# Kernel optimization log

Hardware: AMD Instinct MI355X
Metric: run time of the kernel (lower is better)

Reference implementation:

```python
import jax, jax.numpy as jnp
import numpy as np

N = 100000
E = 1000000
HID = 64


def gcn_conv(x, W, b, edge_index, edge_w, num_nodes):
    # PyG GCNConv with edge_weight: add self-loops (weight 1), symmetric norm,
    # out[c] = sum_e norm_e * (x @ W)[row_e] aggregated at col_e, plus bias.
    xw = x @ W  # [N, hid]
    row = jnp.concatenate([edge_index[0], jnp.arange(num_nodes)])
    col = jnp.concatenate([edge_index[1], jnp.arange(num_nodes)])
    ew = jnp.concatenate([edge_w, jnp.ones((num_nodes,), x.dtype)])
    deg = jax.ops.segment_sum(ew, col, num_segments=num_nodes)
    dinv = jnp.where(deg > 0, jax.lax.rsqrt(deg), 0.0)
    norm = dinv[row] * ew * dinv[col]  # [E+N]
    msgs = norm[:, None] * xw[row]  # [E+N, hid]
    out = jax.ops.segment_sum(msgs, col, num_segments=num_nodes)
    return out + b


def setup_inputs() -> dict:
    key = jax.random.key(0)
    ks = jax.random.split(key, 12)
    user_x = jax.random.normal(ks[0], (N, 3), jnp.float32)
    movie_x = jax.random.normal(ks[1], (N, 18), jnp.float32)
    edge_index = jax.random.randint(ks[2], (2, E), 0, N, jnp.int64)
    edge_attr = jax.random.uniform(ks[3], (E,), jnp.float32)
    def lin(k, fan_in, fan_out):
        bound = 1.0 / np.sqrt(fan_in)
        k1, k2 = jax.random.split(k)
        W = jax.random.uniform(k1, (fan_in, fan_out), jnp.float32, -bound, bound)
        b = jax.random.uniform(k2, (fan_out,), jnp.float32, -bound, bound)
        return W, b
    W_user, b_user = lin(ks[4], 3, HID)
    W_movie, b_movie = lin(ks[5], 18, HID)
    W1, b1 = lin(ks[6], 2 * HID, 128)
    W2, b2 = lin(ks[7], 128, 1)
    return {"user_x": user_x, "movie_x": movie_x, "edge_index": edge_index,
            "edge_attr": edge_attr, "W_user": W_user, "b_user": b_user,
            "W_movie": W_movie, "b_movie": b_movie, "W1": W1, "b1": b1,
            "W2": W2, "b2": b2}


def reference(user_x, movie_x, edge_index, edge_attr, W_user, b_user,
              W_movie, b_movie, W1, b1, W2, b2):
    user_out = gcn_conv(user_x, W_user, b_user, edge_index, edge_attr, N)
    movie_out = gcn_conv(movie_x, W_movie, b_movie, edge_index, edge_attr, N)
    h = jnp.concatenate([user_out, movie_out], axis=-1)  # [N, 128]
    h = jax.nn.relu(h @ W1 + b1)
    rating_pred = h @ W2 + b2  # [N, 1]
    return rating_pred
```

## Files before the change

### kernel.cpp

```cpp
#include <hip/hip_runtime.h>
#include <hip/hip_fp16.h>

#define NN 100000
#define NE 1000000
#define BSH 7
#define BCOLS 128
#define NBUCK 782
#define SBLK 256
#define SITER 16
#define CAP 2048
#define OVCAP 16384

__device__ __forceinline__ float2 h2f(unsigned u) {
    union { unsigned u; __half2 h; } c; c.u = u;
    return __half22float2(c.h);
}
__device__ __forceinline__ unsigned f2h2(float a, float b) {
    union { __half2 h; unsigned u; } c; c.h = __floats2half2_rn(a, b);
    return c.u;
}

#define ACC_ROW16(base)                                                      \
    {                                                                        \
        const uint4* pr_ = (const uint4*)(base);                             \
        const uint4 A_ = pr_[0];                                             \
        const uint4 B_ = pr_[1];                                             \
        const uint4 C_ = pr_[2];                                             \
        float2 f_;                                                           \
        f_ = h2f(A_.x); s21[0]  = fmaf(w, f_.x, s21[0]);  s21[1]  = fmaf(w, f_.y, s21[1]);  \
        f_ = h2f(A_.y); s21[2]  = fmaf(w, f_.x, s21[2]);  s21[3]  = fmaf(w, f_.y, s21[3]);  \
        f_ = h2f(A_.z); s21[4]  = fmaf(w, f_.x, s21[4]);  s21[5]  = fmaf(w, f_.y, s21[5]);  \
        f_ = h2f(A_.w); s21[6]  = fmaf(w, f_.x, s21[6]);  s21[7]  = fmaf(w, f_.y, s21[7]);  \
        f_ = h2f(B_.x); s21[8]  = fmaf(w, f_.x, s21[8]);  s21[9]  = fmaf(w, f_.y, s21[9]);  \
        f_ = h2f(B_.y); s21[10] = fmaf(w, f_.x, s21[10]); s21[11] = fmaf(w, f_.y, s21[11]); \
        f_ = h2f(B_.z); s21[12] = fmaf(w, f_.x, s21[12]); s21[13] = fmaf(w, f_.y, s21[13]); \
        f_ = h2f(B_.w); s21[14] = fmaf(w, f_.x, s21[14]); s21[15] = fmaf(w, f_.y, s21[15]); \
        f_ = h2f(C_.x); s21[16] = fmaf(w, f_.x, s21[16]); s21[17] = fmaf(w, f_.y, s21[17]); \
        f_ = h2f(C_.y); s21[18] = fmaf(w, f_.x, s21[18]); s21[19] = fmaf(w, f_.y, s21[19]); \
        f_ = h2f(C_.z); s21[20] = fmaf(w, f_.x, s21[20]);                    \
    }

__global__ __launch_bounds__(128) void fuse_kernel(const float* __restrict__ Wu,
                                                   const float* __restrict__ bu,
                                                   const float* __restrict__ Wm,
                                                   const float* __restrict__ bm,
                                                   const float* __restrict__ W1,
                                                   const float* __restrict__ b1,
                                                   const float* __restrict__ W2,
                                                   float* __restrict__ Mt,
                                                   int* __restrict__ gcur,
                                                   int* __restrict__ ovfn) {
    const int j = threadIdx.x;
    for (int i = j; i < NBUCK; i += 128) gcur[i] = 0;
    if (j == 0) *ovfn = 0;

    float w1c[128];
#pragma unroll
    for (int k = 0; k < 128; k++) w1c[k] = W1[k * 128 + j];

    float* row = Mt + j * 24;
#pragma unroll
    for (int m = 0; m < 3; m++) {
        float acc = 0.f;
#pragma unroll
        for (int k = 0; k < 64; k++) acc = fmaf(Wu[m * 64 + k], w1c[k], acc);
        row[m] = acc;
    }
#pragma unroll
    for (int m = 0; m < 18; m++) {
        float acc = 0.f;
#pragma unroll
        for (int k = 0; k < 64; k++) acc = fmaf(Wm[m * 64 + k], w1c[64 + k], acc);
        row[3 + m] = acc;
    }
    float bp = b1[j];
#pragma unroll
    for (int k = 0; k < 64; k++) {
        bp = fmaf(bu[k], w1c[k], bp);
        bp = fmaf(bm[k], w1c[64 + k], bp);
    }
    row[21] = bp;
    row[22] = W2[j];
    row[23] = 0.f;
}

__global__ __launch_bounds__(256) void bscatter_kernel(const int* __restrict__ ei,
                                                       const float* __restrict__ ew,
                                                       int* __restrict__ gcur,
                                                       int2* __restrict__ mid,
                                                       int4* __restrict__ ovf,
                                                       int* __restrict__ ovfn) {
    __shared__ int h[NBUCK];
    __shared__ int rbase[NBUCK];
    int cs[SITER], rs[SITER];
    float wv[SITER];
    const int e0 = blockIdx.x * 256 + threadIdx.x;

    for (int i = threadIdx.x; i < NBUCK; i += 256) h[i] = 0;
    __syncthreads();
#pragma unroll
    for (int k = 0; k < SITER; k++) {
        const int e = e0 + k * (SBLK * 256);
        if (e < NE) {
            cs[k] = ei[NE + e];
            rs[k] = ei[e];
            wv[k] = ew[e];
            atomicAdd(&h[cs[k] >> BSH], 1);
        }
    }
    __syncthreads();
    for (int i = threadIdx.x; i < NBUCK; i += 256) {
        const int c0 = h[i];
        rbase[i] = c0 ? atomicAdd(&gcur[i], c0) : 0;
        h[i] = 0;
    }
    __syncthreads();
#pragma unroll
    for (int k = 0; k < SITER; k++) {
        const int e = e0 + k * (SBLK * 256);
        if (e < NE) {
            const int bb = cs[k] >> BSH;
            const int pos = rbase[bb] + atomicAdd(&h[bb], 1);
            if (pos < CAP) {
                mid[(size_t)bb * CAP + pos] =
                    make_int2((cs[k] & (BCOLS - 1)) | (rs[k] << BSH),
                              __float_as_int(wv[k]));
            } else {
                const int oi = atomicAdd(ovfn, 1);
                if (oi < OVCAP)
                    ovf[oi] = make_int4(cs[k], rs[k], __float_as_int(wv[k]), 0);
            }
        }
    }
}

__global__ __launch_bounds__(256) void bdeg_pack_kernel(const int2* __restrict__ mid,
                                                        const int* __restrict__ gcur,
                                                        const int* __restrict__ ovfn,
                                                        const int4* __restrict__ ovf,
                                                        const float* __restrict__ ux,
                                                        const float* __restrict__ mx,
                                                        unsigned short* __restrict__ pack16,
                                                        float* __restrict__ dinv) {
    __shared__ float dl[BCOLS];
    const int b = blockIdx.x;
    const int t = threadIdx.x;
    if (t < BCOLS) dl[t] = 0.f;
    __syncthreads();
    const int cntt = gcur[b];
    const int segc = cntt < CAP ? cntt : CAP;
    const int start = b * CAP;
    for (int i = t; i < segc; i += 256) {
        const int2 p = mid[start + i];
        atomicAdd(&dl[p.x & (BCOLS - 1)], __int_as_float(p.y));
    }
    if (cntt > CAP) {
        const int n = min(*ovfn, OVCAP);
        for (int i = t; i < n; i += 256) {
            const int4 q = ovf[i];
            if ((q.x >> BSH) == b)
                atomicAdd(&dl[q.x & (BCOLS - 1)], __int_as_float(q.z));
        }
    }
    __syncthreads();
    if (t < BCOLS) {
        const int r = b * BCOLS + t;
        if (r < NN) {
            const float d = rsqrtf(dl[t] + 1.0f);
            dinv[r] = d;
            float v[22];
            const float* u = ux + (size_t)r * 3;
            const float* m = mx + (size_t)r * 18;
            v[0] = d * u[0];
            v[1] = d * u[1];
            v[2] = d * u[2];
#pragma unroll
            for (int k = 0; k < 18; k++) v[3 + k] = d * m[k];
            v[21] = d;
            unsigned wb[16];
#pragma unroll
            for (int k = 0; k < 11; k++) wb[k] = f2h2(v[2 * k], v[2 * k + 1]);
#pragma unroll
            for (int k = 11; k < 16; k++) wb[k] = 0u;
            uint4* dst = (uint4*)(pack16 + (size_t)r * 32);
            dst[0] = make_uint4(wb[0], wb[1], wb[2], wb[3]);
            dst[1] = make_uint4(wb[4], wb[5], wb[6], wb[7]);
            dst[2] = make_uint4(wb[8], wb[9], wb[10], wb[11]);
            dst[3] = make_uint4(wb[12], wb[13], wb[14], wb[15]);
        }
    }
}

__global__ __launch_bounds__(512) void bagg_mlp_kernel(const int2* __restrict__ mid,
                                                       const int* __restrict__ gcur,
                                                       const int* __restrict__ ovfn,
                                                       const int4* __restrict__ ovf,
                                                       const unsigned short* __restrict__ pack16,
                                                       const float* __restrict__ dinv,
                                                       const float* __restrict__ Mt,
                                                       const float* __restrict__ b2,
                                                       float* __restrict__ out) {
    __shared__ int2 smid[CAP];
    __shared__ int ccnt[BCOLS];
    __shared__ int cbase[BCOLS];
    __shared__ int cptr[BCOLS];
    __shared__ float sp[3][BCOLS][21];
    __shared__ float po[3][BCOLS];

    const int b = blockIdx.x;
    const int t = threadIdx.x;
    const int col = t & (BCOLS - 1);
    const int hf = t >> 7;
    const int start = b * CAP;
    const int cntt = gcur[b];
    const int segc = cntt < CAP ? cntt : CAP;

    if (t < BCOLS) ccnt[t] = 0;
    __syncthreads();
    for (int i = t; i < segc; i += 512)
        atomicAdd(&ccnt[mid[start + i].x & (BCOLS - 1)], 1);
    __syncthreads();

    if (t < 64) {
        const int a = ccnt[2 * t];
        const int bb = ccnt[2 * t + 1];
        int p = a + bb;
#pragma unroll
        for (int d = 1; d < 64; d <<= 1) {
            const int x = __shfl_up(p, d, 64);
            if (t >= d) p += x;
        }
        cbase[2 * t] = p - bb;
        cbase[2 * t + 1] = p;
        cptr[2 * t] = p - bb - a;
        cptr[2 * t + 1] = p - bb;
    }
    __syncthreads();

    for (int i = t; i < segc; i += 512) {
        const int2 p = mid[start + i];
        const int pos = atomicAdd(&cptr[p.x & (BCOLS - 1)], 1);
        smid[pos] = p;
    }
    __syncthreads();

    float s21[21];
#pragma unroll
    for (int m = 0; m < 21; m++) s21[m] = 0.f;

    const int s0 = (col == 0) ? 0 : cbase[col - 1];
    const int s1 = cbase[col];
#pragma unroll 2
    for (int i = s0 + hf; i < s1; i += 4) {
        const int2 p = smid[i];
        const unsigned row = ((unsigned)p.x) >> BSH;
        const float w = __int_as_float(p.y);
        ACC_ROW16(pack16 + (size_t)row * 32);
    }

    if (hf) {
#pragma unroll
        for (int m = 0; m < 21; m++) sp[hf - 1][col][m] = s21[m];
    }
    __syncthreads();

    const int c = b * BCOLS + col;
    if (hf == 0) {
#pragma unroll
        for (int m = 0; m < 21; m++)
            s21[m] += sp[0][col][m] + sp[1][col][m] + sp[2][col][m];
        if (cntt > CAP && c < NN) {
            const int n = min(*ovfn, OVCAP);
            for (int i = 0; i < n; i++) {
                const int4 q = ovf[i];
                if (q.x == c) {
                    const unsigned row = (unsigned)q.y;
                    const float w = __int_as_float(q.z);
                    ACC_ROW16(pack16 + (size_t)row * 32);
                }
            }
        }
        if (c < NN) {
            const float w = 1.0f;
            ACC_ROW16(pack16 + (size_t)c * 32);
            const float d = dinv[c];
#pragma unroll
            for (int m = 0; m < 21; m++) s21[m] *= d;
        }
#pragma unroll
        for (int m = 0; m < 21; m++) sp[0][col][m] = s21[m];
    }
    __syncthreads();
    if (hf) {
#pragma unroll
        for (int m = 0; m < 21; m++) s21[m] = sp[0][col][m];
    }

    float o = 0.f;
    if (c < NN) {
        const int k0 = hf * 32;
#pragma unroll 2
        for (int k = k0; k < k0 + 32; k++) {
            const float* r = Mt + k * 24;
            float hsum = r[21];
#pragma unroll
            for (int m = 0; m < 21; m++) hsum = fmaf(s21[m], r[m], hsum);
            o = fmaf(fmaxf(hsum, 0.f), r[22], o);
        }
    }
    if (hf) po[hf - 1][col] = o;
    __syncthreads();
    if (hf == 0 && c < NN)
        out[c] = o + po[0][col] + po[1][col] + po[2][col] + b2[0];
}

extern "C" void kernel_launch(void* const* d_in, const int* in_sizes, int n_in,
                              void* d_out, int out_size, void* d_ws, size_t ws_size,
                              hipStream_t stream) {
    const float* ux = (const float*)d_in[0];
    const float* mx = (const float*)d_in[1];
    const int* ei = (const int*)d_in[2];
    const float* ew = (const float*)d_in[3];
    const float* Wu = (const float*)d_in[4];
    const float* bu = (const float*)d_in[5];
    const float* Wm = (const float*)d_in[6];
    const float* bm = (const float*)d_in[7];
    const float* W1 = (const float*)d_in[8];
    const float* b1 = (const float*)d_in[9];
    const float* W2 = (const float*)d_in[10];
    const float* b2 = (const float*)d_in[11];
    float* out = (float*)d_out;

    char* ws = (char*)d_ws;
    int*            gcur   = (int*)ws;
    int*            ovfn   = (int*)(ws + 4096);
    float*          Mt     = (float*)(ws + 8192);
    float*          dinv   = (float*)(ws + 20480);
    unsigned short* pack16 = (unsigned short*)(ws + 420480);
    int2*           mid    = (int2*)(ws + 6820480);
    int4*           ovf    = (int4*)(ws + 19632768);

    fuse_kernel<<<1, 128, 0, stream>>>(Wu, bu, Wm, bm, W1, b1, W2, Mt, gcur, ovfn);
    bscatter_kernel<<<SBLK, 256, 0, stream>>>(ei, ew, gcur, mid, ovf, ovfn);
    bdeg_pack_kernel<<<NBUCK, 256, 0, stream>>>(mid, gcur, ovfn, ovf, ux, mx, pack16, dinv);
    bagg_mlp_kernel<<<NBUCK, 512, 0, stream>>>(mid, gcur, ovfn, ovf, pack16, dinv, Mt, b2, out);
}
```

Baseline: 185.7 us.

## Split edge aggregation across four threads per column by feature slice

Changes the aggregation thread mapping. Before, four threads each took every fourth edge of a column and read the full 64-byte packed row. Now four adjacent threads each own one 16-byte slice of the packed row and walk all of the column's edges. The aim is coalesced 64-byte row reads across neighbouring lanes, fewer accumulator registers per thread (8 instead of 21), and a cheaper shared-memory reduction. In exchange each thread runs a longer serial loop over a column's edges, and the fourth slice's loads are wasted because that padding is discarded.

```diff
diff --git a/kernel.cpp b/kernel.cpp
--- a/kernel.cpp
+++ b/kernel.cpp
@@ -204,13 +204,11 @@
     __shared__ int ccnt[BCOLS];
     __shared__ int cbase[BCOLS];
     __shared__ int cptr[BCOLS];
-    __shared__ float sp[3][BCOLS][21];
+    __shared__ float sfin[BCOLS][33];
     __shared__ float po[3][BCOLS];
 
     const int b = blockIdx.x;
     const int t = threadIdx.x;
-    const int col = t & (BCOLS - 1);
-    const int hf = t >> 7;
     const int start = b * CAP;
     const int cntt = gcur[b];
     const int segc = cntt < CAP ? cntt : CAP;
@@ -244,58 +242,71 @@
     }
     __syncthreads();
 
-    float s21[21];
-#pragma unroll
-    for (int m = 0; m < 21; m++) s21[m] = 0.f;
-
-    const int s0 = (col == 0) ? 0 : cbase[col - 1];
-    const int s1 = cbase[col];
-#pragma unroll 2
-    for (int i = s0 + hf; i < s1; i += 4) {
-        const int2 p = smid[i];
-        const unsigned row = ((unsigned)p.x) >> BSH;
-        const float w = __int_as_float(p.y);
-        ACC_ROW16(pack16 + (size_t)row * 32);
-    }
-
-    if (hf) {
-#pragma unroll
-        for (int m = 0; m < 21; m++) sp[hf - 1][col][m] = s21[m];
-    }
-    __syncthreads();
-
-    const int c = b * BCOLS + col;
-    if (hf == 0) {
-#pragma unroll
-        for (int m = 0; m < 21; m++)
-            s21[m] += sp[0][col][m] + sp[1][col][m] + sp[2][col][m];
-        if (cntt > CAP && c < NN) {
-            const int n = min(*ovfn, OVCAP);
-            for (int i = 0; i < n; i++) {
-                const int4 q = ovf[i];
-                if (q.x == c) {
-                    const unsigned row = (unsigned)q.y;
-                    const float w = __int_as_float(q.z);
-                    ACC_ROW16(pack16 + (size_t)row * 32);
+    {
+        const int colq = t >> 2;
+        const int slice = t & 3;
+        float sacc[8];
+#pragma unroll
+        for (int m = 0; m < 8; m++) sacc[m] = 0.f;
+
+        const int q0 = (colq == 0) ? 0 : cbase[colq - 1];
+        const int q1 = cbase[colq];
+        const unsigned short* pbase = pack16 + slice * 8;
+#pragma unroll 4
+        for (int i = q0; i < q1; i++) {
+            const int2 p = smid[i];
+            const unsigned row = ((unsigned)p.x) >> BSH;
+            const float w = __int_as_float(p.y);
+            const uint4 Q = *(const uint4*)(pbase + (size_t)row * 32);
+            float2 f;
+            f = h2f(Q.x); sacc[0] = fmaf(w, f.x, sacc[0]); sacc[1] = fmaf(w, f.y, sacc[1]);
+            f = h2f(Q.y); sacc[2] = fmaf(w, f.x, sacc[2]); sacc[3] = fmaf(w, f.y, sacc[3]);
+            f = h2f(Q.z); sacc[4] = fmaf(w, f.x, sacc[4]); sacc[5] = fmaf(w, f.y, sacc[5]);
+            f = h2f(Q.w); sacc[6] = fmaf(w, f.x, sacc[6]); sacc[7] = fmaf(w, f.y, sacc[7]);
+        }
+        if (slice < 3) {
+#pragma unroll
+            for (int m = 0; m < 8; m++) sfin[colq][slice * 8 + m] = sacc[m];
+        }
+    }
+    __syncthreads();
+
+    {
+        const int colq = t >> 2;
+        const int slice = t & 3;
+        const int cc = b * BCOLS + colq;
+        if (slice == 0 && cc < NN) {
+            float s21[21];
+#pragma unroll
+            for (int m = 0; m < 21; m++) s21[m] = sfin[colq][m];
+            if (cntt > CAP) {
+                const int n = min(*ovfn, OVCAP);
+                for (int i = 0; i < n; i++) {
+                    const int4 q = ovf[i];
+                    if (q.x == cc) {
+                        const unsigned row = (unsigned)q.y;
+                        const float w = __int_as_float(q.z);
+                        ACC_ROW16(pack16 + (size_t)row * 32);
+                    }
                 }
             }
-        }
-        if (c < NN) {
-            const float w = 1.0f;
-            ACC_ROW16(pack16 + (size_t)c * 32);
-            const float d = dinv[c];
-#pragma unroll
-            for (int m = 0; m < 21; m++) s21[m] *= d;
-        }
-#pragma unroll
-        for (int m = 0; m < 21; m++) sp[0][col][m] = s21[m];
-    }
-    __syncthreads();
-    if (hf) {
-#pragma unroll
-        for (int m = 0; m < 21; m++) s21[m] = sp[0][col][m];
-    }
-
+            {
+                const float w = 1.0f;
+                ACC_ROW16(pack16 + (size_t)cc * 32);
+            }
+            const float d = dinv[cc];
+#pragma unroll
+            for (int m = 0; m < 21; m++) sfin[colq][m] = s21[m] * d;
+        }
+    }
+    __syncthreads();
+
+    const int col = t & (BCOLS - 1);
+    const int hf = t >> 7;
+    const int c = b * BCOLS + col;
+    float s21[21];
+#pragma unroll
+    for (int m = 0; m < 21; m++) s21[m] = sfin[col][m];
     float o = 0.f;
     if (c < NN) {
         const int k0 = hf * 32;
```

New measurement: 182.0 us, median of 2. 1.02x faster.
